# Optimization experiments

Hardware: AMD Instinct MI355X
Metric: run time of the kernel (lower is better)

## Reference

```python
import jax, jax.numpy as jnp
import numpy as np

N_HEAD = 16
MAX_WAVELENGTH = 10000
ROPE_PCT = 1.0


def apply_p_rope(inputs, positions, head_dim, max_wavelength=MAX_WAVELENGTH, rope_percentage=ROPE_PCT):
    # inputs: [..., T, D], positions: [T]
    rope_angles = int(rope_percentage * head_dim // 2)
    nope_angles = head_dim // 2 - rope_angles
    fraction = 2.0 * jnp.arange(0, rope_angles) / head_dim
    timescale = max_wavelength ** fraction
    timescale = jnp.pad(timescale, (0, nope_angles), mode='constant', constant_values=(0, jnp.inf))
    sinusoid_inp = positions[..., None] / timescale[None, :]  # [T, D/2]
    sin = jnp.sin(sinusoid_inp)
    cos = jnp.cos(sinusoid_inp)
    first_half, second_half = jnp.split(inputs, 2, axis=-1)
    first_part = first_half * cos - second_half * sin
    second_part = second_half * cos + first_half * sin
    return jnp.concatenate([first_part, second_part], axis=-1).astype(inputs.dtype)


def setup_inputs() -> dict:
    key = jax.random.key(0)
    ks = jax.random.split(key, 4)
    B, T, C = 2, 2048, 1024
    x = jax.random.normal(ks[0], (B, T, C), dtype=jnp.float32)
    W_attn = jax.random.normal(ks[1], (C, 3 * C), dtype=jnp.float32) * 0.02
    b_attn = jnp.zeros((3 * C,), dtype=jnp.float32)
    W_proj = jax.random.normal(ks[2], (C, C), dtype=jnp.float32) * 0.02
    b_proj = jnp.zeros((C,), dtype=jnp.float32)
    return {"x": x, "W_attn": W_attn, "b_attn": b_attn, "W_proj": W_proj, "b_proj": b_proj}


def reference(x, W_attn, b_attn, W_proj, b_proj):
    B, T, C = x.shape
    H = N_HEAD
    D = C // H  # head_dim
    qkv = x @ W_attn + b_attn                     # [B, T, 3C]
    q, k, v = jnp.split(qkv, 3, axis=-1)
    def split_heads(t):
        return t.reshape(B, T, H, D).transpose(0, 2, 1, 3)  # [B, H, T, D]
    q, k, v = split_heads(q), split_heads(k), split_heads(v)
    positions = jnp.arange(T, dtype=q.dtype)
    q = apply_p_rope(q, positions, D)
    k = apply_p_rope(k, positions, D)
    scale = jnp.sqrt(D).astype(k.dtype)
    attn = jnp.einsum('bhqd,bhkd->bhqk', q, k) / scale  # [B, H, T, T]
    causal_mask = jnp.tril(jnp.ones((T, T))).astype(bool)
    attn = jnp.where(causal_mask, attn, jnp.finfo(attn.dtype).min)
    attn = jax.nn.softmax(attn, axis=-1)
    y = jnp.einsum('bhqk,bhkd->bhqd', attn, v)    # [B, H, T, D]
    y = y.transpose(0, 2, 1, 3).reshape(B, T, C)
    return y @ W_proj + b_proj
```

## Files before the change

kernel.cpp:

```cpp
#include <hip/hip_runtime.h>
#include <hip/hip_bf16.h>

typedef short short8 __attribute__((ext_vector_type(8)));
typedef float f32x4 __attribute__((ext_vector_type(4)));
typedef __hip_bfloat16 bf16;

#define MFMA(a, b, c) __builtin_amdgcn_mfma_f32_16x16x32_bf16(a, b, c, 0, 0, 0)
#define EXP2(x) __builtin_amdgcn_exp2f(x)

__device__ __forceinline__ void async16(const void* g, void* l) {
  __builtin_amdgcn_global_load_lds((const __attribute__((address_space(1))) void*)g,
                                   (__attribute__((address_space(3))) void*)l, 16, 0, 0);
}

__device__ __forceinline__ short f2bs(float x) {
  bf16 h = __float2bfloat16(x);
  return __builtin_bit_cast(short, h);
}
__device__ __forceinline__ unsigned pk2(float lo, float hi) {
  return ((unsigned)(unsigned short)f2bs(hi) << 16) | (unsigned)(unsigned short)f2bs(lo);
}

__launch_bounds__(256)
__global__ void prep(const float* __restrict__ Wa, bf16* __restrict__ WaT,
                     const float* __restrict__ Wp, bf16* __restrict__ WpT,
                     const float* __restrict__ x, bf16* __restrict__ xb,
                     float2* __restrict__ tab) {
  __shared__ __align__(16) short Ts[64 * 72];
  int id = blockIdx.x;
  int tid = threadIdx.x;
  if (id < 1024) {
    const float* src; bf16* dst; int R, Cc, bx, by;
    if (id < 768) { src = Wa; dst = WaT; R = 1024; Cc = 3072; bx = id % 48; by = id / 48; }
    else { int r = id - 768; src = Wp; dst = WpT; R = 1024; Cc = 1024; bx = r & 15; by = r >> 4; }
    int r0 = by * 64, c0 = bx * 64;
#pragma unroll
    for (int c = 0; c < 4; ++c) {
      int g = c * 1024 + tid * 4;
      int rr = g >> 6, cc = g & 63;
      float4 v = *(const float4*)(src + (size_t)(r0 + rr) * Cc + c0 + cc);
      Ts[rr * 72 + cc + 0] = f2bs(v.x);
      Ts[rr * 72 + cc + 1] = f2bs(v.y);
      Ts[rr * 72 + cc + 2] = f2bs(v.z);
      Ts[rr * 72 + cc + 3] = f2bs(v.w);
    }
    __syncthreads();
#pragma unroll
    for (int c = 0; c < 2; ++c) {
      int g = c * 2048 + tid * 8;
      int co = g >> 6, ro = g & 63;
      short8 vv;
#pragma unroll
      for (int jj = 0; jj < 8; ++jj) vv[jj] = Ts[(ro + jj) * 72 + co];
      *(short8*)(dst + (size_t)(c0 + co) * R + r0 + ro) = vv;
    }
  } else {
    int cid = id - 1024;
    int i0 = (cid * 256 + tid) * 8;
    float4 a = *(const float4*)(x + i0);
    float4 b = *(const float4*)(x + i0 + 4);
    short8 o;
    o[0] = f2bs(a.x); o[1] = f2bs(a.y); o[2] = f2bs(a.z); o[3] = f2bs(a.w);
    o[4] = f2bs(b.x); o[5] = f2bs(b.y); o[6] = f2bs(b.z); o[7] = f2bs(b.w);
    *(short8*)((short*)xb + i0) = o;
    if (cid < 256) {
      int idx = cid * 256 + tid;
      int t = idx >> 5, d = idx & 31;
      float inv = powf(10000.0f, -(float)d * (1.0f / 32.0f));
      float ang = (float)t * inv;
      tab[idx] = make_float2(cosf(ang), sinf(ang));
    }
  }
}

__launch_bounds__(256)
__global__ void gemm_qkv(const bf16* __restrict__ A, const bf16* __restrict__ Bt,
                         const float* __restrict__ bias,
                         const float2* __restrict__ rope,
                         bf16* __restrict__ qp, bf16* __restrict__ kp,
                         bf16* __restrict__ vp) {
  const int K = 1024;
  __shared__ __align__(16) short As[128 * 32];
  __shared__ __align__(16) short Bs[128 * 32];
  int tid = threadIdx.x;
  int lane = tid & 63, wave = tid >> 6;
  int l = lane & 15, quad = lane >> 4;
  int wm = wave & 1, wn = wave >> 1;
  int mBase = blockIdx.y * 128, nBase = blockIdx.x * 128;

  f32x4 acc[4][4] = {};

  int r0 = tid >> 2;
  int kk = (tid & 3) * 8;
  const bf16* Ap = A + (size_t)(mBase + r0) * K + kk;
  const bf16* Bp = Bt + (size_t)(nBase + r0) * K + kk;
  short* Asp = As + tid * 8;
  short* Bsp = Bs + tid * 8;

  for (int kb = 0; kb < K / 32; ++kb) {
    __syncthreads();
    async16(Ap, Asp);
    async16(Ap + (size_t)64 * K, Asp + 2048);
    async16(Bp, Bsp);
    async16(Bp + (size_t)64 * K, Bsp + 2048);
    Ap += 32; Bp += 32;
    __syncthreads();
    short8 af[4], bfr[4];
#pragma unroll
    for (int i = 0; i < 4; ++i)
      af[i] = *(const short8*)(As + (wm * 64 + i * 16 + l) * 32 + quad * 8);
#pragma unroll
    for (int j = 0; j < 4; ++j)
      bfr[j] = *(const short8*)(Bs + (wn * 64 + j * 16 + l) * 32 + quad * 8);
#pragma unroll
    for (int i = 0; i < 4; ++i)
#pragma unroll
      for (int j = 0; j < 4; ++j)
        acc[i][j] = MFMA(af[i], bfr[j], acc[i][j]);
  }

  int nsec = nBase + wn * 64;
  float bv[4];
#pragma unroll
  for (int j = 0; j < 4; ++j) bv[j] = bias[nsec + j * 16 + l];

  int sel = nsec >> 10;
  int h = (nsec & 1023) >> 6;
  if (sel < 2) {
    bf16* dst = (sel == 0) ? qp : kp;
    float mul = (sel == 0) ? 0.18033688f : 1.0f;
#pragma unroll
    for (int i = 0; i < 4; ++i) {
#pragma unroll
      for (int reg = 0; reg < 4; ++reg) {
        int m = mBase + wm * 64 + i * 16 + quad * 4 + reg;
        int t = m & 2047, b = m >> 11;
        size_t base = ((size_t)((b * 16 + h) * 2048 + t)) * 64;
#pragma unroll
        for (int j = 0; j < 2; ++j) {
          int d = j * 16 + l;
          float x1 = acc[i][j][reg] + bv[j];
          float x2 = acc[i][j + 2][reg] + bv[j + 2];
          float2 cs = rope[t * 32 + d];
          dst[base + d]      = __float2bfloat16((x1 * cs.x - x2 * cs.y) * mul);
          dst[base + d + 32] = __float2bfloat16((x2 * cs.x + x1 * cs.y) * mul);
        }
      }
    }
  } else {
#pragma unroll
    for (int i = 0; i < 4; ++i) {
      int m0 = mBase + wm * 64 + i * 16 + quad * 4;
      int t0 = m0 & 2047, b = m0 >> 11;
#pragma unroll
      for (int j = 0; j < 4; ++j) {
        int d = j * 16 + l;
        uint2 uu;
        uu.x = pk2(acc[i][j][0] + bv[j], acc[i][j][1] + bv[j]);
        uu.y = pk2(acc[i][j][2] + bv[j], acc[i][j][3] + bv[j]);
        *(uint2*)(vp + ((size_t)((b * 16 + h) * 64 + d)) * 2048 + t0) = uu;
      }
    }
  }
}

__launch_bounds__(256)
__global__ void gemm_proj(const bf16* __restrict__ A, const bf16* __restrict__ Bt,
                          const float* __restrict__ bias, float* __restrict__ out) {
  const int K = 1024, Nn = 1024;
  __shared__ __align__(16) short As[64 * 32];
  __shared__ __align__(16) short Bs[128 * 32];
  int tid = threadIdx.x;
  int lane = tid & 63, wave = tid >> 6;
  int l = lane & 15, quad = lane >> 4;
  int mBase = blockIdx.y * 64, nBase = blockIdx.x * 128;

  f32x4 acc[4][2] = {};

  int r0 = tid >> 2;
  int kk = (tid & 3) * 8;
  const bf16* Ap = A + (size_t)(mBase + r0) * K + kk;
  const bf16* Bp = Bt + (size_t)(nBase + r0) * K + kk;
  short* Asp = As + tid * 8;
  short* Bsp = Bs + tid * 8;

  for (int kb = 0; kb < K / 32; ++kb) {
    __syncthreads();
    async16(Ap, Asp);
    async16(Bp, Bsp);
    async16(Bp + (size_t)64 * K, Bsp + 2048);
    Ap += 32; Bp += 32;
    __syncthreads();
    short8 af[4], bfr[2];
#pragma unroll
    for (int i = 0; i < 4; ++i)
      af[i] = *(const short8*)(As + (i * 16 + l) * 32 + quad * 8);
#pragma unroll
    for (int j = 0; j < 2; ++j)
      bfr[j] = *(const short8*)(Bs + (wave * 32 + j * 16 + l) * 32 + quad * 8);
#pragma unroll
    for (int i = 0; i < 4; ++i)
#pragma unroll
      for (int j = 0; j < 2; ++j)
        acc[i][j] = MFMA(af[i], bfr[j], acc[i][j]);
  }

  int nsec = nBase + wave * 32;
  float bv[2];
#pragma unroll
  for (int j = 0; j < 2; ++j) bv[j] = bias[nsec + j * 16 + l];
#pragma unroll
  for (int i = 0; i < 4; ++i)
#pragma unroll
    for (int reg = 0; reg < 4; ++reg) {
      int m = mBase + i * 16 + quad * 4 + reg;
#pragma unroll
      for (int j = 0; j < 2; ++j)
        out[(size_t)m * Nn + nsec + j * 16 + l] = acc[i][j][reg] + bv[j];
    }
}

__launch_bounds__(256)
__global__ void flash_attn(const bf16* __restrict__ q, const bf16* __restrict__ k,
                           const bf16* __restrict__ vt, bf16* __restrict__ y) {
  __shared__ __align__(16) short Ps[4 * 32 * 66];
  int tid = threadIdx.x;
  int lane = tid & 63, wave = tid >> 6;
  int l = lane & 15, quad = lane >> 4;
  int bh = blockIdx.x;
  int by = blockIdx.y;
  int qi = (by < 8) ? (15 - by) : (by - 8);
  int q0 = qi * 128;
  int bb = bh >> 4, hh = bh & 15;

  const bf16* qh = q + (size_t)bh * 2048 * 64;
  const bf16* kh = k + (size_t)bh * 2048 * 64;
  const bf16* vh = vt + (size_t)bh * 64 * 2048;

  int qrb = q0 + wave * 32;

  short8 qf[2][2];
#pragma unroll
  for (int m = 0; m < 2; ++m)
#pragma unroll
    for (int ks = 0; ks < 2; ++ks)
      qf[m][ks] = *(const short8*)(qh + (size_t)(qrb + m * 16 + l) * 64 + ks * 32 + quad * 8);

  const bf16* kfp = kh + (size_t)l * 64 + quad * 8;
  const bf16* vfp = vh + (size_t)l * 2048 + quad * 8;

  f32x4 acc[2][4] = {};
  float lr[2][4] = {{0.f, 0.f, 0.f, 0.f}, {0.f, 0.f, 0.f, 0.f}};
  short* Pw = Ps + wave * (32 * 66);
  int nkt = ((qrb + 31) >> 6) + 1;

  for (int kt = 0; kt < nkt; ++kt) {
    int kv0 = kt * 64;

    short8 kf[2][4];
#pragma unroll
    for (int ks = 0; ks < 2; ++ks)
#pragma unroll
      for (int jn = 0; jn < 4; ++jn)
        kf[ks][jn] = *(const short8*)(kfp + (size_t)(kv0 + jn * 16) * 64 + ks * 32);

    f32x4 sacc[2][4];
#pragma unroll
    for (int m = 0; m < 2; ++m)
#pragma unroll
      for (int jn = 0; jn < 4; ++jn) sacc[m][jn] = f32x4{-16.f, -16.f, -16.f, -16.f};
    bool live1 = (kv0 <= qrb + 31);
#pragma unroll
    for (int ks = 0; ks < 2; ++ks)
#pragma unroll
      for (int jn = 0; jn < 4; ++jn) {
        sacc[0][jn] = MFMA(qf[0][ks], kf[ks][jn], sacc[0][jn]);
        sacc[1][jn] = MFMA(qf[1][ks], kf[ks][jn], sacc[1][jn]);
      }

    short8 vf[2][4];
#pragma unroll
    for (int ks = 0; ks < 2; ++ks)
#pragma unroll
      for (int jd = 0; jd < 4; ++jd)
        vf[ks][jd] = *(const short8*)(vfp + (size_t)(jd * 16) * 2048 + kv0 + ks * 32);

#pragma unroll
    for (int m = 0; m < 2; ++m) {
      int qlo = qrb + m * 16;
      if (m == 0 && kv0 > qlo + 15) continue;
      bool nm = (kv0 + 63) > qlo;
#pragma unroll
      for (int reg = 0; reg < 4; ++reg) {
        int qg = qlo + quad * 4 + reg;
        int prow = (m * 16 + quad * 4 + reg) * 66 + l;
        float ps = 0.f;
#pragma unroll
        for (int jn = 0; jn < 4; ++jn) {
          float s = sacc[m][jn][reg];
          if (nm) s = (kv0 + jn * 16 + l <= qg) ? s : -1e30f;
          float p = EXP2(s);
          ps += p;
          Pw[prow + jn * 16] = f2bs(p);
        }
        lr[m][reg] += ps;
      }
    }

#pragma unroll
    for (int m = 0; m < 2; ++m) {
      if (m == 0 && kv0 > qrb + 15) continue;
      if (m == 1 && !live1) continue;
#pragma unroll
      for (int ks = 0; ks < 2; ++ks) {
        short8 pf = *(const short8*)(Pw + (m * 16 + l) * 66 + ks * 32 + quad * 8);
#pragma unroll
        for (int jd = 0; jd < 4; ++jd)
          acc[m][jd] = MFMA(pf, vf[ks][jd], acc[m][jd]);
      }
    }
  }

#pragma unroll
  for (int m = 0; m < 2; ++m) {
#pragma unroll
    for (int reg = 0; reg < 4; ++reg) {
      float s = lr[m][reg];
#pragma unroll
      for (int mm = 1; mm <= 8; mm <<= 1)
        s += __shfl_xor(s, mm, 64);
      float inv = 1.0f / s;
      int t = qrb + m * 16 + quad * 4 + reg;
      size_t yb = ((size_t)(bb * 2048 + t)) * 1024 + hh * 64;
#pragma unroll
      for (int jd = 0; jd < 4; ++jd)
        y[yb + jd * 16 + l] = __float2bfloat16(acc[m][jd][reg] * inv);
    }
  }
}

extern "C" void kernel_launch(void* const* d_in, const int* in_sizes, int n_in,
                              void* d_out, int out_size, void* d_ws, size_t ws_size,
                              hipStream_t stream) {
  const float* x  = (const float*)d_in[0];
  const float* Wa = (const float*)d_in[1];
  const float* ba = (const float*)d_in[2];
  const float* Wp = (const float*)d_in[3];
  const float* bp = (const float*)d_in[4];

  char* ws = (char*)d_ws;
  bf16*   WaT  = (bf16*)(ws);
  bf16*   WpT  = (bf16*)(ws + 6291456);
  float2* rope = (float2*)(ws + 8388608);
  bf16*   xb   = (bf16*)(ws + 8913152);
  bf16*   qw   = xb + 4194304;
  bf16*   kw   = qw + 4194304;
  bf16*   vtw  = kw + 4194304;
  bf16*   yw   = vtw + 4194304;

  prep<<<3072, 256, 0, stream>>>(Wa, WaT, Wp, WpT, x, xb, rope);
  gemm_qkv<<<dim3(24, 32), 256, 0, stream>>>(xb, WaT, ba, rope, qw, kw, vtw);
  flash_attn<<<dim3(32, 16), 256, 0, stream>>>(qw, kw, vtw, yw);
  gemm_proj<<<dim3(8, 64), 256, 0, stream>>>(yw, WpT, bp, (float*)d_out);
}
```

Baseline: 215.9 us.

## Rewrite flash attention with 32x32 MFMA and register-resident P via lane shuffles

Switches the attention kernel from 16x16x32 to 32x32x16 bf16 MFMA tiles and computes the score tile transposed (K as the A operand), so each lane holds one query's probabilities. The P matrix now moves to the PV MFMA layout with cross-half lane shuffles instead of an LDS round trip, and the causal loop steps in 32-key blocks so only the last block needs masking. The aim is to remove LDS traffic and masking overhead and to issue fewer, larger MFMAs. In exchange the kernel issues more global load instructions per key tile and keeps a longer serial MFMA dependency chain per wave.

```diff
diff --git a/kernel.cpp b/kernel.cpp
--- a/kernel.cpp
+++ b/kernel.cpp
@@ -3,9 +3,11 @@
 
 typedef short short8 __attribute__((ext_vector_type(8)));
 typedef float f32x4 __attribute__((ext_vector_type(4)));
+typedef float f32x16 __attribute__((ext_vector_type(16)));
 typedef __hip_bfloat16 bf16;
 
 #define MFMA(a, b, c) __builtin_amdgcn_mfma_f32_16x16x32_bf16(a, b, c, 0, 0, 0)
+#define MFMA32(a, b, c) __builtin_amdgcn_mfma_f32_32x32x16_bf16(a, b, c, 0, 0, 0)
 #define EXP2(x) __builtin_amdgcn_exp2f(x)
 
 __device__ __forceinline__ void async16(const void* g, void* l) {
@@ -223,119 +225,108 @@
 __launch_bounds__(256)
 __global__ void flash_attn(const bf16* __restrict__ q, const bf16* __restrict__ k,
                            const bf16* __restrict__ vt, bf16* __restrict__ y) {
-  __shared__ __align__(16) short Ps[4 * 32 * 66];
   int tid = threadIdx.x;
   int lane = tid & 63, wave = tid >> 6;
-  int l = lane & 15, quad = lane >> 4;
+  int l32 = lane & 31, hi = lane >> 5;
   int bh = blockIdx.x;
   int by = blockIdx.y;
   int qi = (by < 8) ? (15 - by) : (by - 8);
   int q0 = qi * 128;
   int bb = bh >> 4, hh = bh & 15;
+  int qrb = q0 + wave * 32;
 
   const bf16* qh = q + (size_t)bh * 2048 * 64;
   const bf16* kh = k + (size_t)bh * 2048 * 64;
   const bf16* vh = vt + (size_t)bh * 64 * 2048;
 
-  int qrb = q0 + wave * 32;
-
-  short8 qf[2][2];
-#pragma unroll
-  for (int m = 0; m < 2; ++m)
-#pragma unroll
-    for (int ks = 0; ks < 2; ++ks)
-      qf[m][ks] = *(const short8*)(qh + (size_t)(qrb + m * 16 + l) * 64 + ks * 32 + quad * 8);
-
-  const bf16* kfp = kh + (size_t)l * 64 + quad * 8;
-  const bf16* vfp = vh + (size_t)l * 2048 + quad * 8;
-
-  f32x4 acc[2][4] = {};
-  float lr[2][4] = {{0.f, 0.f, 0.f, 0.f}, {0.f, 0.f, 0.f, 0.f}};
-  short* Pw = Ps + wave * (32 * 66);
-  int nkt = ((qrb + 31) >> 6) + 1;
-
-  for (int kt = 0; kt < nkt; ++kt) {
-    int kv0 = kt * 64;
-
-    short8 kf[2][4];
-#pragma unroll
-    for (int ks = 0; ks < 2; ++ks)
-#pragma unroll
-      for (int jn = 0; jn < 4; ++jn)
-        kf[ks][jn] = *(const short8*)(kfp + (size_t)(kv0 + jn * 16) * 64 + ks * 32);
-
-    f32x4 sacc[2][4];
-#pragma unroll
-    for (int m = 0; m < 2; ++m)
-#pragma unroll
-      for (int jn = 0; jn < 4; ++jn) sacc[m][jn] = f32x4{-16.f, -16.f, -16.f, -16.f};
-    bool live1 = (kv0 <= qrb + 31);
-#pragma unroll
-    for (int ks = 0; ks < 2; ++ks)
-#pragma unroll
-      for (int jn = 0; jn < 4; ++jn) {
-        sacc[0][jn] = MFMA(qf[0][ks], kf[ks][jn], sacc[0][jn]);
-        sacc[1][jn] = MFMA(qf[1][ks], kf[ks][jn], sacc[1][jn]);
+  short8 qf[4];
+#pragma unroll
+  for (int d16 = 0; d16 < 4; ++d16)
+    qf[d16] = *(const short8*)(qh + (size_t)(qrb + l32) * 64 + d16 * 16 + hi * 8);
+
+  const bf16* kfp = kh + (size_t)l32 * 64 + hi * 8;
+  const bf16* vfp = vh + (size_t)l32 * 2048 + hi * 8;
+
+  f32x16 acc0, acc1;
+#pragma unroll
+  for (int i = 0; i < 16; ++i) { acc0[i] = 0.f; acc1[i] = 0.f; }
+  float lr = 0.f;
+
+  int n32 = (qrb >> 5) + 1;
+
+  for (int kt = 0; kt < n32; ++kt) {
+    int kv0 = kt * 32;
+
+    short8 kf[4];
+#pragma unroll
+    for (int d16 = 0; d16 < 4; ++d16)
+      kf[d16] = *(const short8*)(kfp + (size_t)kv0 * 64 + d16 * 16);
+
+    f32x16 sacc;
+#pragma unroll
+    for (int i = 0; i < 16; ++i) sacc[i] = -16.f;
+#pragma unroll
+    for (int d16 = 0; d16 < 4; ++d16)
+      sacc = MFMA32(kf[d16], qf[d16], sacc);
+
+    float p[16];
+    bool diag = (kt == n32 - 1);
+#pragma unroll
+    for (int r = 0; r < 16; ++r) {
+      float s = sacc[r];
+      if (diag) {
+        int kvl = (r & 3) + 8 * (r >> 2) + 4 * hi;
+        s = (kvl <= l32) ? s : -1e30f;
       }
-
-    short8 vf[2][4];
-#pragma unroll
-    for (int ks = 0; ks < 2; ++ks)
-#pragma unroll
-      for (int jd = 0; jd < 4; ++jd)
-        vf[ks][jd] = *(const short8*)(vfp + (size_t)(jd * 16) * 2048 + kv0 + ks * 32);
-
-#pragma unroll
-    for (int m = 0; m < 2; ++m) {
-      int qlo = qrb + m * 16;
-      if (m == 0 && kv0 > qlo + 15) continue;
-      bool nm = (kv0 + 63) > qlo;
-#pragma unroll
-      for (int reg = 0; reg < 4; ++reg) {
-        int qg = qlo + quad * 4 + reg;
-        int prow = (m * 16 + quad * 4 + reg) * 66 + l;
-        float ps = 0.f;
-#pragma unroll
-        for (int jn = 0; jn < 4; ++jn) {
-          float s = sacc[m][jn][reg];
-          if (nm) s = (kv0 + jn * 16 + l <= qg) ? s : -1e30f;
-          float p = EXP2(s);
-          ps += p;
-          Pw[prow + jn * 16] = f2bs(p);
-        }
-        lr[m][reg] += ps;
-      }
-    }
-
-#pragma unroll
-    for (int m = 0; m < 2; ++m) {
-      if (m == 0 && kv0 > qrb + 15) continue;
-      if (m == 1 && !live1) continue;
-#pragma unroll
-      for (int ks = 0; ks < 2; ++ks) {
-        short8 pf = *(const short8*)(Pw + (m * 16 + l) * 66 + ks * 32 + quad * 8);
-#pragma unroll
-        for (int jd = 0; jd < 4; ++jd)
-          acc[m][jd] = MFMA(pf, vf[ks][jd], acc[m][jd]);
-      }
-    }
-  }
-
-#pragma unroll
-  for (int m = 0; m < 2; ++m) {
-#pragma unroll
-    for (int reg = 0; reg < 4; ++reg) {
-      float s = lr[m][reg];
-#pragma unroll
-      for (int mm = 1; mm <= 8; mm <<= 1)
-        s += __shfl_xor(s, mm, 64);
-      float inv = 1.0f / s;
-      int t = qrb + m * 16 + quad * 4 + reg;
-      size_t yb = ((size_t)(bb * 2048 + t)) * 1024 + hh * 64;
-#pragma unroll
-      for (int jd = 0; jd < 4; ++jd)
-        y[yb + jd * 16 + l] = __float2bfloat16(acc[m][jd][reg] * inv);
-    }
+      p[r] = EXP2(s);
+    }
+    float ps = 0.f;
+#pragma unroll
+    for (int r = 0; r < 16; ++r) ps += p[r];
+    lr += ps;
+
+    unsigned Pk[4][2];
+#pragma unroll
+    for (int r2 = 0; r2 < 4; ++r2) {
+      Pk[r2][0] = pk2(p[4 * r2 + 0], p[4 * r2 + 1]);
+      Pk[r2][1] = pk2(p[4 * r2 + 2], p[4 * r2 + 3]);
+    }
+
+#pragma unroll
+    for (int s = 0; s < 2; ++s) {
+      unsigned E0 = hi ? Pk[2 * s][0] : Pk[2 * s + 1][0];
+      unsigned E1 = hi ? Pk[2 * s][1] : Pk[2 * s + 1][1];
+      unsigned O0 = hi ? Pk[2 * s + 1][0] : Pk[2 * s][0];
+      unsigned O1 = hi ? Pk[2 * s + 1][1] : Pk[2 * s][1];
+      unsigned pE0 = (unsigned)__shfl_xor((int)E0, 32, 64);
+      unsigned pE1 = (unsigned)__shfl_xor((int)E1, 32, 64);
+      int4 wz;
+      wz.x = (int)(hi ? pE0 : O0);
+      wz.y = (int)(hi ? pE1 : O1);
+      wz.z = (int)(hi ? O0 : pE0);
+      wz.w = (int)(hi ? O1 : pE1);
+      short8 pfrag = __builtin_bit_cast(short8, wz);
+
+      short8 vf0 = *(const short8*)(vfp + kv0 + s * 16);
+      short8 vf1 = *(const short8*)(vfp + (size_t)32 * 2048 + kv0 + s * 16);
+      acc0 = MFMA32(vf0, pfrag, acc0);
+      acc1 = MFMA32(vf1, pfrag, acc1);
+    }
+  }
+
+  lr += __shfl_xor(lr, 32, 64);
+  float inv = 1.0f / lr;
+
+  size_t ybase = ((size_t)(bb * 2048 + qrb + l32)) * 1024 + hh * 64;
+#pragma unroll
+  for (int r2 = 0; r2 < 4; ++r2) {
+    uint2 u0, u1;
+    u0.x = pk2(acc0[4 * r2 + 0] * inv, acc0[4 * r2 + 1] * inv);
+    u0.y = pk2(acc0[4 * r2 + 2] * inv, acc0[4 * r2 + 3] * inv);
+    u1.x = pk2(acc1[4 * r2 + 0] * inv, acc1[4 * r2 + 1] * inv);
+    u1.y = pk2(acc1[4 * r2 + 2] * inv, acc1[4 * r2 + 3] * inv);
+    *(uint2*)(y + ybase + 8 * r2 + 4 * hi)      = u0;
+    *(uint2*)(y + ybase + 32 + 8 * r2 + 4 * hi) = u1;
   }
 }
 
```

After: 220.5 us. +2.1%, slower.
